# Performance work log

Measured on AMD Instinct MI355X. Metric: run time of the kernel, lower is better.

Reference implementation:

```python
import jax, jax.numpy as jnp
import numpy as np

NUM_HEADS = 16

def setup_inputs() -> dict:
    key = jax.random.key(0)
    k_x, k_wq, k_bq, k_wo, k_bo = jax.random.split(key, 5)
    B, S, D = 4, 2048, 1024
    x = jax.random.normal(k_x, (B, S, D), dtype=jnp.float32)
    # Flax Dense default init: lecun_normal for kernel, zeros for bias; use small normals here.
    w_qkv = jax.random.normal(k_wq, (D, 3 * D), dtype=jnp.float32) * (D ** -0.5)
    b_qkv = jnp.zeros((3 * D,), dtype=jnp.float32)
    w_out = jax.random.normal(k_wo, (D, D), dtype=jnp.float32) * (D ** -0.5)
    b_out = jnp.zeros((D,), dtype=jnp.float32)
    return {"x": x, "w_qkv": w_qkv, "b_qkv": b_qkv, "w_out": w_out, "b_out": b_out}

def reference(x, w_qkv, b_qkv, w_out, b_out):
    B, S, D = x.shape
    H = NUM_HEADS
    hd = D // H
    scale = hd ** -0.5
    qkv = x @ w_qkv + b_qkv                                  # [B,S,3D]
    qkv = qkv.reshape(B, S, 3, H, hd)
    qkv = jnp.transpose(qkv, (2, 0, 3, 1, 4))                # [3,B,H,S,hd]
    q, k, v = qkv[0], qkv[1], qkv[2]
    attn = jnp.einsum("bhqd,bhkd->bhqk", q, k) * scale       # [B,H,S,S]
    attn = jax.nn.softmax(attn, axis=-1)
    out = jnp.einsum("bhqk,bhkd->bhqd", attn, v)             # [B,H,S,hd]
    out = jnp.transpose(out, (0, 2, 1, 3)).reshape(B, S, D)
    return out @ w_out + b_out
```

## Files before the change

kernel.cpp:

```cpp
#include <hip/hip_runtime.h>
#include <cstdint>
#include <cstddef>

#define B_    4
#define S_    2048
#define D_    1024
#define H_    16
#define HD_   64
#define M_    8192
#define NQKV  3072

typedef __bf16 bf16;
typedef __bf16 bf16x4 __attribute__((ext_vector_type(4)));
typedef __bf16 bf16x8 __attribute__((ext_vector_type(8)));
typedef float  f32x2  __attribute__((ext_vector_type(2)));
typedef float  f32x4  __attribute__((ext_vector_type(4)));
typedef float  f32x16 __attribute__((ext_vector_type(16)));
typedef unsigned short u16x4 __attribute__((ext_vector_type(4)));
typedef uint32_t u32x2 __attribute__((ext_vector_type(2)));
typedef uint32_t u32x4 __attribute__((ext_vector_type(4)));

__device__ __forceinline__ void gl2lds16(const void* g, void* l) {
  __builtin_amdgcn_global_load_lds(
      (__attribute__((address_space(1))) void*)(uintptr_t)g,
      (__attribute__((address_space(3))) void*)l, 16, 0, 0);
}

__device__ __forceinline__ uint32_t pkbf16(float a, float b) {
  union { bf16 h[2]; uint32_t u; } z;
  z.h[0] = (bf16)a; z.h[1] = (bf16)b;
  return z.u;
}

__global__ __launch_bounds__(256) void cast_f32_bf16(const float* __restrict__ in,
                                                     bf16* __restrict__ out, int n4) {
  int i = blockIdx.x * 256 + threadIdx.x;
  if (i >= n4) return;
  float4 v = ((const float4*)in)[i];
  bf16x4 o;
  o[0] = (bf16)v.x; o[1] = (bf16)v.y; o[2] = (bf16)v.z; o[3] = (bf16)v.w;
  ((bf16x4*)out)[i] = o;
}

__global__ __launch_bounds__(256) void transpose_cast(const float* __restrict__ in,
                                                      bf16* __restrict__ out, int R, int C) {
  __shared__ float tile[32][33];
  int bx = blockIdx.x * 32, by = blockIdx.y * 32;
  int tx = threadIdx.x, ty = threadIdx.y;
#pragma unroll
  for (int i = 0; i < 32; i += 8)
    tile[ty + i][tx] = in[(size_t)(by + ty + i) * C + bx + tx];
  __syncthreads();
#pragma unroll
  for (int i = 0; i < 32; i += 8)
    out[(size_t)(bx + ty + i) * R + by + tx] = (bf16)tile[tx][ty + i];
}

template <bool OUT_BF16>
__global__ __launch_bounds__(256) void gemm_bt(const bf16* __restrict__ A,
                                               const bf16* __restrict__ Bt,
                                               const float* __restrict__ bias,
                                               void* __restrict__ Cptr,
                                               int M, int N, int K) {
  __shared__ __align__(16) bf16 As[128 * 64];
  __shared__ __align__(16) bf16 Bs[128 * 64];
  const int tid  = threadIdx.x;
  const int lane = tid & 63, w = tid >> 6;
  const int lo   = lane & 15, quad = lane >> 4;
  const int xcd = blockIdx.x & 7, g = blockIdx.x >> 3;
  const int mi  = g & 7,          n = g >> 3;
  const int bm  = (xcd * 8 + mi) * 128, bn = n * 128;
  const int wm = (w >> 1) * 64,    wn = (w & 1) * 64;

  f32x4 acc[4][4];
  const f32x4 zero = {0.f, 0.f, 0.f, 0.f};
#pragma unroll
  for (int i = 0; i < 4; ++i)
#pragma unroll
    for (int j = 0; j < 4; ++j) acc[i][j] = zero;

  for (int k0 = 0; k0 < K; k0 += 64) {
#pragma unroll
    for (int c = 0; c < 4; ++c) {
      int seg = c * 4 + w;
      int idx = seg * 512 + lane * 8;
      int row = idx >> 6, col = idx & 63;
      gl2lds16(A  + (size_t)(bm + row) * K + k0 + col, As + seg * 512);
      gl2lds16(Bt + (size_t)(bn + row) * K + k0 + col, Bs + seg * 512);
    }
    __syncthreads();
#pragma unroll
    for (int ks = 0; ks < 2; ++ks) {
      bf16x8 av[4], bv[4];
#pragma unroll
      for (int i = 0; i < 4; ++i)
        av[i] = *(const bf16x8*)&As[(wm + i * 16 + lo) * 64 + ks * 32 + quad * 8];
#pragma unroll
      for (int j = 0; j < 4; ++j)
        bv[j] = *(const bf16x8*)&Bs[(wn + j * 16 + lo) * 64 + ks * 32 + quad * 8];
#pragma unroll
      for (int i = 0; i < 4; ++i)
#pragma unroll
        for (int j = 0; j < 4; ++j)
          acc[i][j] = __builtin_amdgcn_mfma_f32_16x16x32_bf16(av[i], bv[j], acc[i][j], 0, 0, 0);
    }
    __syncthreads();
  }
#pragma unroll
  for (int j = 0; j < 4; ++j) {
    int cg = bn + wn + j * 16 + lo;
    float bsv = bias[cg];
#pragma unroll
    for (int i = 0; i < 4; ++i) {
      int rg = bm + wm + i * 16 + quad * 4;
#pragma unroll
      for (int r = 0; r < 4; ++r) {
        float v = acc[i][j][r] + bsv;
        if (OUT_BF16) ((bf16*)Cptr)[(size_t)(rg + r) * N + cg] = (bf16)v;
        else          ((float*)Cptr)[(size_t)(rg + r) * N + cg] = v;
      }
    }
  }
}

__global__ __launch_bounds__(256, 2) void gemm_bt_wide(const bf16* __restrict__ A,
                                                       const bf16* __restrict__ Bt,
                                                       const float* __restrict__ bias,
                                                       bf16* __restrict__ Cptr,
                                                       int M, int N, int K) {
  __shared__ __align__(16) bf16 As[128 * 64];
  __shared__ __align__(16) bf16 Bs[256 * 64];
  const int tid  = threadIdx.x;
  const int lane = tid & 63, w = tid >> 6;
  const int lo   = lane & 15, quad = lane >> 4;
  const int xcd = blockIdx.x & 7, g = blockIdx.x >> 3;
  const int mi  = g & 7,          n = g >> 3;
  const int bm  = (xcd * 8 + mi) * 128, bn = n * 256;
  const int wm = (w >> 1) * 64,    wn = (w & 1) * 128;

  f32x4 acc[4][8];
  const f32x4 zero = {0.f, 0.f, 0.f, 0.f};
#pragma unroll
  for (int i = 0; i < 4; ++i)
#pragma unroll
    for (int j = 0; j < 8; ++j) acc[i][j] = zero;

  for (int k0 = 0; k0 < K; k0 += 64) {
#pragma unroll
    for (int c = 0; c < 4; ++c) {
      int seg = c * 4 + w;
      int idx = seg * 512 + lane * 8;
      int row = idx >> 6, col = idx & 63;
      gl2lds16(A + (size_t)(bm + row) * K + k0 + col, As + seg * 512);
    }
#pragma unroll
    for (int c = 0; c < 8; ++c) {
      int seg = c * 4 + w;
      int idx = seg * 512 + lane * 8;
      int row = idx >> 6, col = idx & 63;
      gl2lds16(Bt + (size_t)(bn + row) * K + k0 + col, Bs + seg * 512);
    }
    __syncthreads();
#pragma unroll
    for (int ks = 0; ks < 2; ++ks) {
      bf16x8 av[4], bv[8];
#pragma unroll
      for (int i = 0; i < 4; ++i)
        av[i] = *(const bf16x8*)&As[(wm + i * 16 + lo) * 64 + ks * 32 + quad * 8];
#pragma unroll
      for (int j = 0; j < 8; ++j)
        bv[j] = *(const bf16x8*)&Bs[(wn + j * 16 + lo) * 64 + ks * 32 + quad * 8];
#pragma unroll
      for (int i = 0; i < 4; ++i)
#pragma unroll
        for (int j = 0; j < 8; ++j)
          acc[i][j] = __builtin_amdgcn_mfma_f32_16x16x32_bf16(av[i], bv[j], acc[i][j], 0, 0, 0);
    }
    __syncthreads();
  }
#pragma unroll
  for (int j = 0; j < 8; ++j) {
    int cg = bn + wn + j * 16 + lo;
    float bsv = bias[cg];
#pragma unroll
    for (int i = 0; i < 4; ++i) {
      int rg = bm + wm + i * 16 + quad * 4;
#pragma unroll
      for (int r = 0; r < 4; ++r)
        Cptr[(size_t)(rg + r) * N + cg] = (bf16)(acc[i][j][r] + bsv);
    }
  }
}

__global__ __launch_bounds__(256, 2) void flash_attn(const bf16* __restrict__ qkv,
                                                     bf16* __restrict__ out) {
  __shared__ __align__(16) bf16 smem[16384];
  bf16* const Ksm = smem;
  bf16* const Vsm = smem + 8192;

  const int tid  = threadIdx.x;
  const int lane = tid & 63, wq = tid >> 6;
  const int l31  = lane & 31;
  const int e    = lane >> 5;
  const int hi8  = e * 8, hi4 = e * 4;

  const int bid = blockIdx.x;
  const int qb  = bid >> 6;
  const int bh  = bid & 63;
  const int h   = bh & 15;
  const int b   = bh >> 4;
  const int q0  = qb * 256;
  const size_t rowb = (size_t)b * S_;
  const bf16* qbase = qkv + rowb * NQKV + h * HD_;
  const bf16* kbase = qbase + D_;
  const bf16* vbase = qbase + 2 * D_;

  bf16x8 qfA[4], qfB[4];
  {
    const bf16* qrow0 = qbase + (size_t)(q0 + wq * 64 + l31) * NQKV;
    const bf16* qrow1 = qrow0 + (size_t)32 * NQKV;
#pragma unroll
    for (int c = 0; c < 4; ++c) {
      qfA[c] = *(const bf16x8*)(qrow0 + c * 16 + hi8);
      qfB[c] = *(const bf16x8*)(qrow1 + c * 16 + hi8);
    }
  }

  int kq_off[2];
#pragma unroll
  for (int it = 0; it < 2; ++it) {
    int ci = it * 256 + tid;
    int s  = ci >> 3;
    int x  = (ci & 7) ^ (s & 7);
    kq_off[it] = s * NQKV + x * 8;
  }
  int vs_d[2], vs_s[2], vs_off[2];
#pragma unroll
  for (int u = 0; u < 2; ++u) {
    int idx = u * 256 + tid;
    int d0 = (idx & 31) * 2;
    int s0 = (idx >> 5) * 4;
    vs_d[u] = d0;
    vs_s[u] = s0;
    vs_off[u] = (((s0 >> 3) ^ ((d0 >> 1) & 7)) * 8) + (s0 & 7);
  }

  uint32_t vreg[2][4];

#pragma unroll
  for (int it = 0; it < 2; ++it)
    gl2lds16(kbase + kq_off[it], Ksm + (it * 256 + wq * 64) * 8);
#pragma unroll
  for (int u = 0; u < 2; ++u)
#pragma unroll
    for (int j = 0; j < 4; ++j)
      vreg[u][j] = *(const uint32_t*)(vbase + (size_t)(vs_s[u] + j) * NQKV + vs_d[u]);

  const f32x16 zero16 = {0.f,0.f,0.f,0.f,0.f,0.f,0.f,0.f,0.f,0.f,0.f,0.f,0.f,0.f,0.f,0.f};
  f32x16 oacc[2][2];
  oacc[0][0] = zero16; oacc[0][1] = zero16;
  oacc[1][0] = zero16; oacc[1][1] = zero16;
  f32x2 psA = {0.f, 0.f}, psB = {0.f, 0.f};
  const float c2 = 0.125f * 1.44269504088896341f;

  for (int kt = 0; kt < 32; ++kt) {
    const int buf = kt & 1;
#pragma unroll
    for (int u = 0; u < 2; ++u) {
      int d0 = vs_d[u];
      uint32_t lo0 = __builtin_amdgcn_perm(vreg[u][1], vreg[u][0], 0x05040100u);
      uint32_t lo1 = __builtin_amdgcn_perm(vreg[u][3], vreg[u][2], 0x05040100u);
      uint32_t hi0 = __builtin_amdgcn_perm(vreg[u][1], vreg[u][0], 0x07060302u);
      uint32_t hi1 = __builtin_amdgcn_perm(vreg[u][3], vreg[u][2], 0x07060302u);
      u32x2 lov = {lo0, lo1}, hiv = {hi0, hi1};
      *(u32x2*)&Vsm[buf * 4096 + (d0 + 0) * 64 + vs_off[u]] = lov;
      *(u32x2*)&Vsm[buf * 4096 + (d0 + 1) * 64 + vs_off[u]] = hiv;
    }
    __syncthreads();

    {
      int ktn = (kt + 1 < 32) ? kt + 1 : 31;
      const bf16* kb = kbase + (size_t)ktn * 64 * NQKV;
#pragma unroll
      for (int it = 0; it < 2; ++it)
        gl2lds16(kb + kq_off[it], Ksm + (buf ^ 1) * 4096 + (it * 256 + wq * 64) * 8);
    }
    {
      int ktn = (kt + 1 < 32) ? kt + 1 : 31;
      const bf16* vb = vbase + (size_t)ktn * 64 * NQKV;
#pragma unroll
      for (int u = 0; u < 2; ++u)
#pragma unroll
        for (int j = 0; j < 4; ++j)
          vreg[u][j] = *(const uint32_t*)(vb + (size_t)(vs_s[u] + j) * NQKV + vs_d[u]);
    }

#pragma unroll
    for (int kk = 0; kk < 2; ++kk) {
      f32x16 sA = zero16, sB = zero16;
      int srow = kk * 32 + l31;
      int swz  = (srow & 7) * 8;
#pragma unroll
      for (int c = 0; c < 4; ++c) {
        bf16x8 kf = *(const bf16x8*)&Ksm[buf * 4096 + srow * 64 + ((c * 16 + hi8) ^ swz)];
        sA = __builtin_amdgcn_mfma_f32_32x32x16_bf16(kf, qfA[c], sA, 0, 0, 0);
        sB = __builtin_amdgcn_mfma_f32_32x32x16_bf16(kf, qfB[c], sB, 0, 0, 0);
      }

      uint32_t Q8a[8], Q8b[8];
#pragma unroll
      for (int i = 0; i < 8; ++i) {
        f32x2 sva, svb;
        sva[0] = sA[2 * i]; sva[1] = sA[2 * i + 1];
        svb[0] = sB[2 * i]; svb[1] = sB[2 * i + 1];
        f32x2 ta = sva * c2 - 16.0f;
        f32x2 tb = svb * c2 - 16.0f;
        float a0 = __builtin_amdgcn_exp2f(ta[0]);
        float a1 = __builtin_amdgcn_exp2f(ta[1]);
        float b0 = __builtin_amdgcn_exp2f(tb[0]);
        float b1 = __builtin_amdgcn_exp2f(tb[1]);
        psA += (f32x2){a0, a1};
        psB += (f32x2){b0, b1};
        Q8a[i] = pkbf16(a0, a1);
        Q8b[i] = pkbf16(b0, b1);
      }

#pragma unroll
      for (int mh = 0; mh < 2; ++mh) {
        const int m = kk * 2 + mh, bq = mh * 4;
        u32x4 pda, pdb;
#if __has_builtin(__builtin_amdgcn_permlane32_swap)
        u32x2 wa0 = __builtin_amdgcn_permlane32_swap(Q8a[bq],     Q8a[bq + 2], false, false);
        u32x2 wa1 = __builtin_amdgcn_permlane32_swap(Q8a[bq + 1], Q8a[bq + 3], false, false);
        pda[0] = wa0[0]; pda[1] = wa1[0]; pda[2] = wa0[1]; pda[3] = wa1[1];
        u32x2 wb0 = __builtin_amdgcn_permlane32_swap(Q8b[bq],     Q8b[bq + 2], false, false);
        u32x2 wb1 = __builtin_amdgcn_permlane32_swap(Q8b[bq + 1], Q8b[bq + 3], false, false);
        pdb[0] = wb0[0]; pdb[1] = wb1[0]; pdb[2] = wb0[1]; pdb[3] = wb1[1];
#else
        {
          uint32_t s0 = e ? Q8a[bq]     : Q8a[bq + 2];
          uint32_t s1 = e ? Q8a[bq + 1] : Q8a[bq + 3];
          uint32_t r0 = __shfl_xor(s0, 32);
          uint32_t r1 = __shfl_xor(s1, 32);
          pda[0] = e ? r0 : Q8a[bq];
          pda[1] = e ? r1 : Q8a[bq + 1];
          pda[2] = e ? Q8a[bq + 2] : r0;
          pda[3] = e ? Q8a[bq + 3] : r1;
        }
        {
          uint32_t s0 = e ? Q8b[bq]     : Q8b[bq + 2];
          uint32_t s1 = e ? Q8b[bq + 1] : Q8b[bq + 3];
          uint32_t r0 = __shfl_xor(s0, 32);
          uint32_t r1 = __shfl_xor(s1, 32);
          pdb[0] = e ? r0 : Q8b[bq];
          pdb[1] = e ? r1 : Q8b[bq + 1];
          pdb[2] = e ? Q8b[bq + 2] : r0;
          pdb[3] = e ? Q8b[bq + 3] : r1;
        }
#endif
        bf16x8 pfa = __builtin_bit_cast(bf16x8, pda);
        bf16x8 pfb = __builtin_bit_cast(bf16x8, pdb);
#pragma unroll
        for (int dt = 0; dt < 2; ++dt) {
          int drow = dt * 32 + l31;
          int swv  = (drow >> 1) & 7;
          bf16x8 vf = *(const bf16x8*)&Vsm[buf * 4096 + drow * 64 + (((m * 2 + e) ^ swv) * 8)];
          oacc[dt][0] = __builtin_amdgcn_mfma_f32_32x32x16_bf16(vf, pfa, oacc[dt][0], 0, 0, 0);
          oacc[dt][1] = __builtin_amdgcn_mfma_f32_32x32x16_bf16(vf, pfb, oacc[dt][1], 0, 0, 0);
        }
      }
    }
  }

  float lsumA = psA[0] + psA[1];
  float lsumB = psB[0] + psB[1];
  lsumA += __shfl_xor(lsumA, 32);
  lsumB += __shfl_xor(lsumB, 32);

  __syncthreads();
  bf16* Os = smem;
  {
    float invA = 1.f / lsumA;
    float invB = 1.f / lsumB;
#pragma unroll
    for (int qs = 0; qs < 2; ++qs) {
      float inv = qs ? invB : invA;
      int ql = wq * 64 + qs * 32 + l31;
      int swO = (ql >> 1) & 7;
#pragma unroll
      for (int dt = 0; dt < 2; ++dt) {
#pragma unroll
        for (int g = 0; g < 4; ++g) {
          bf16x4 ov;
#pragma unroll
          for (int jj = 0; jj < 4; ++jj)
            ov[jj] = (bf16)(oacc[dt][qs][g * 4 + jj] * inv);
          *(bf16x4*)&Os[ql * 64 + (((dt * 4 + g) ^ swO) * 8) + hi4] = ov;
        }
      }
    }
  }
  __syncthreads();
#pragma unroll
  for (int it = 0; it < 8; ++it) {
    int idx = it * 256 + tid;
    int row = idx >> 3, c8 = idx & 7;
    bf16x8 t = *(const bf16x8*)&Os[row * 64 + ((c8 ^ ((row >> 1) & 7)) * 8)];
    *(bf16x8*)&out[(rowb + q0 + row) * D_ + h * HD_ + c8 * 8] = t;
  }
}

extern "C" void kernel_launch(void* const* d_in, const int* in_sizes, int n_in,
                              void* d_out, int out_size, void* d_ws, size_t ws_size,
                              hipStream_t stream) {
  const float* x     = (const float*)d_in[0];
  const float* w_qkv = (const float*)d_in[1];
  const float* b_qkv = (const float*)d_in[2];
  const float* w_out = (const float*)d_in[3];
  const float* b_out = (const float*)d_in[4];
  float* out = (float*)d_out;

  char* ws = (char*)d_ws;
  bf16* xb    = (bf16*)(ws);
  bf16* wqkvT = (bf16*)(ws + (size_t)16777216);
  bf16* woutT = (bf16*)(ws + (size_t)23068672);
  bf16* qkvb  = (bf16*)(ws + (size_t)25165824);
  bf16* attnb = (bf16*)(ws + (size_t)75497472);

  cast_f32_bf16<<<(M_ * D_ / 4 + 255) / 256, 256, 0, stream>>>(x, xb, M_ * D_ / 4);
  transpose_cast<<<dim3(NQKV / 32, D_ / 32), dim3(32, 8), 0, stream>>>(w_qkv, wqkvT, D_, NQKV);
  transpose_cast<<<dim3(D_ / 32, D_ / 32), dim3(32, 8), 0, stream>>>(w_out, woutT, D_, D_);

  gemm_bt_wide<<<(M_ / 128) * (NQKV / 256), 256, 0, stream>>>(
      xb, wqkvT, b_qkv, qkvb, M_, NQKV, D_);

  flash_attn<<<B_ * H_ * (S_ / 256), 256, 0, stream>>>(qkvb, attnb);

  gemm_bt<false><<<(M_ / 128) * (D_ / 128), 256, 0, stream>>>(
      attnb, woutT, b_out, (void*)out, M_, D_, D_);
}
```

Baseline: 283.2 us.

## Replace both GEMMs with triple-buffered 256x128 swizzled pipelined kernel and add MFMA priority

Both projection GEMMs now use one new kernel with 512 threads and a 256x128 output tile. It keeps a three-stage ring of tiles in LDS with an XOR swizzle. Global-to-LDS loads for the tile two steps ahead are split across the four MFMA phases and gated by vmcnt waits and barriers. This is meant to hide load latency and avoid LDS bank conflicts. s_setprio is also raised around the MFMA sections in both the GEMM and the flash attention kernel. The cost is 144KB of dynamic LDS, which allows only one block per CU, plus more frequent barriers.

```diff
diff --git a/kernel.cpp b/kernel.cpp
--- a/kernel.cpp
+++ b/kernel.cpp
@@ -16,9 +16,10 @@
 typedef float  f32x2  __attribute__((ext_vector_type(2)));
 typedef float  f32x4  __attribute__((ext_vector_type(4)));
 typedef float  f32x16 __attribute__((ext_vector_type(16)));
-typedef unsigned short u16x4 __attribute__((ext_vector_type(4)));
 typedef uint32_t u32x2 __attribute__((ext_vector_type(2)));
 typedef uint32_t u32x4 __attribute__((ext_vector_type(4)));
+
+#define MFMA16(a, b, c) __builtin_amdgcn_mfma_f32_16x16x32_bf16(a, b, c, 0, 0, 0)
 
 __device__ __forceinline__ void gl2lds16(const void* g, void* l) {
   __builtin_amdgcn_global_load_lds(
@@ -57,20 +58,41 @@
 }
 
 template <bool OUT_BF16>
-__global__ __launch_bounds__(256) void gemm_bt(const bf16* __restrict__ A,
-                                               const bf16* __restrict__ Bt,
-                                               const float* __restrict__ bias,
-                                               void* __restrict__ Cptr,
-                                               int M, int N, int K) {
-  __shared__ __align__(16) bf16 As[128 * 64];
-  __shared__ __align__(16) bf16 Bs[128 * 64];
+__global__ __launch_bounds__(512, 2) void gemm256(const bf16* __restrict__ A,
+                                                  const bf16* __restrict__ Bt,
+                                                  const float* __restrict__ bias,
+                                                  void* __restrict__ Cptr,
+                                                  int M, int N, int K) {
+  extern __shared__ __align__(16) bf16 sm[];
   const int tid  = threadIdx.x;
   const int lane = tid & 63, w = tid >> 6;
   const int lo   = lane & 15, quad = lane >> 4;
-  const int xcd = blockIdx.x & 7, g = blockIdx.x >> 3;
-  const int mi  = g & 7,          n = g >> 3;
-  const int bm  = (xcd * 8 + mi) * 128, bn = n * 128;
-  const int wm = (w >> 1) * 64,    wn = (w & 1) * 64;
+  const int wr   = w >> 1, wc = w & 1;
+  const int xcd  = blockIdx.x & 7, g = blockIdx.x >> 3;
+  const int mi_  = g & 3, n_ = g >> 2;
+  const int bm   = (xcd * 4 + mi_) * 256, bn = n_ * 128;
+
+  const bf16* Ag = A  + (size_t)bm * K;
+  const bf16* Bg = Bt + (size_t)bn * K;
+
+  const int swzl  = lo & 7;
+  const int laneA = (wr * 64 + lo) * 64;
+  const int laneB = (wc * 64 + lo) * 64;
+  const int pc0   = (quad ^ swzl) * 8;
+  const int pc1   = ((4 + quad) ^ swzl) * 8;
+
+  int aoffG[4], boffG[2];
+#pragma unroll
+  for (int la = 0; la < 4; ++la) {
+    int ca = la * 512 + tid, row = ca >> 3, s = ca & 7;
+    aoffG[la] = row * K + ((s ^ (row & 7)) * 8);
+  }
+#pragma unroll
+  for (int lb = 0; lb < 2; ++lb) {
+    int cb = lb * 512 + tid, row = cb >> 3, s = cb & 7;
+    boffG[lb] = row * K + ((s ^ (row & 7)) * 8);
+  }
+  const int T = K >> 6;
 
   f32x4 acc[4][4];
   const f32x4 zero = {0.f, 0.f, 0.f, 0.f};
@@ -79,115 +101,116 @@
 #pragma unroll
     for (int j = 0; j < 4; ++j) acc[i][j] = zero;
 
-  for (int k0 = 0; k0 < K; k0 += 64) {
-#pragma unroll
-    for (int c = 0; c < 4; ++c) {
-      int seg = c * 4 + w;
-      int idx = seg * 512 + lane * 8;
-      int row = idx >> 6, col = idx & 63;
-      gl2lds16(A  + (size_t)(bm + row) * K + k0 + col, As + seg * 512);
-      gl2lds16(Bt + (size_t)(bn + row) * K + k0 + col, Bs + seg * 512);
-    }
-    __syncthreads();
-#pragma unroll
-    for (int ks = 0; ks < 2; ++ks) {
-      bf16x8 av[4], bv[4];
-#pragma unroll
-      for (int i = 0; i < 4; ++i)
-        av[i] = *(const bf16x8*)&As[(wm + i * 16 + lo) * 64 + ks * 32 + quad * 8];
-#pragma unroll
-      for (int j = 0; j < 4; ++j)
-        bv[j] = *(const bf16x8*)&Bs[(wn + j * 16 + lo) * 64 + ks * 32 + quad * 8];
-#pragma unroll
-      for (int i = 0; i < 4; ++i)
-#pragma unroll
-        for (int j = 0; j < 4; ++j)
-          acc[i][j] = __builtin_amdgcn_mfma_f32_16x16x32_bf16(av[i], bv[j], acc[i][j], 0, 0, 0);
-    }
-    __syncthreads();
-  }
+#pragma unroll
+  for (int la = 0; la < 4; ++la)
+    gl2lds16(Ag + aoffG[la], sm + (la * 512 + tid) * 8);
+#pragma unroll
+  for (int lb = 0; lb < 2; ++lb)
+    gl2lds16(Bg + boffG[lb], sm + 16384 + (lb * 512 + tid) * 8);
+#pragma unroll
+  for (int la = 0; la < 4; ++la)
+    gl2lds16(Ag + 64 + aoffG[la], sm + 24576 + (la * 512 + tid) * 8);
+#pragma unroll
+  for (int lb = 0; lb < 2; ++lb)
+    gl2lds16(Bg + 64 + boffG[lb], sm + 24576 + 16384 + (lb * 512 + tid) * 8);
+  asm volatile("s_waitcnt vmcnt(6)" ::: "memory");
+  __builtin_amdgcn_s_barrier();
+
+  auto body = [&](int t, bool st) __attribute__((always_inline)) {
+    bf16* As_ = sm + (t % 3) * 24576;
+    bf16* Bs_ = As_ + 16384;
+    bf16* An_ = sm + ((t + 2) % 3) * 24576;
+    bf16* Bn_ = An_ + 16384;
+    const size_t kg = (size_t)(t + 2) * 64;
+    bf16x8 av0, av1, bv[4];
+
+    av0 = *(const bf16x8*)&As_[laneA + 0 * 1024 + pc0];
+    av1 = *(const bf16x8*)&As_[laneA + 1 * 1024 + pc0];
+#pragma unroll
+    for (int j = 0; j < 4; ++j)
+      bv[j] = *(const bf16x8*)&Bs_[laneB + j * 1024 + pc0];
+    if (st) {
+      gl2lds16(Ag + kg + aoffG[0], An_ + (0 * 512 + tid) * 8);
+      gl2lds16(Ag + kg + aoffG[1], An_ + (1 * 512 + tid) * 8);
+    }
+    __builtin_amdgcn_s_barrier();
+    __builtin_amdgcn_s_setprio(1);
+#pragma unroll
+    for (int j = 0; j < 4; ++j) {
+      acc[0][j] = MFMA16(av0, bv[j], acc[0][j]);
+      acc[1][j] = MFMA16(av1, bv[j], acc[1][j]);
+    }
+    __builtin_amdgcn_s_setprio(0);
+
+    av0 = *(const bf16x8*)&As_[laneA + 2 * 1024 + pc0];
+    av1 = *(const bf16x8*)&As_[laneA + 3 * 1024 + pc0];
+    if (st) {
+      gl2lds16(Ag + kg + aoffG[2], An_ + (2 * 512 + tid) * 8);
+      gl2lds16(Ag + kg + aoffG[3], An_ + (3 * 512 + tid) * 8);
+    }
+    __builtin_amdgcn_s_barrier();
+    __builtin_amdgcn_s_setprio(1);
+#pragma unroll
+    for (int j = 0; j < 4; ++j) {
+      acc[2][j] = MFMA16(av0, bv[j], acc[2][j]);
+      acc[3][j] = MFMA16(av1, bv[j], acc[3][j]);
+    }
+    __builtin_amdgcn_s_setprio(0);
+
+    av0 = *(const bf16x8*)&As_[laneA + 0 * 1024 + pc1];
+    av1 = *(const bf16x8*)&As_[laneA + 1 * 1024 + pc1];
+#pragma unroll
+    for (int j = 0; j < 4; ++j)
+      bv[j] = *(const bf16x8*)&Bs_[laneB + j * 1024 + pc1];
+    if (st)
+      gl2lds16(Bg + kg + boffG[0], Bn_ + (0 * 512 + tid) * 8);
+    __builtin_amdgcn_s_barrier();
+    __builtin_amdgcn_s_setprio(1);
+#pragma unroll
+    for (int j = 0; j < 4; ++j) {
+      acc[0][j] = MFMA16(av0, bv[j], acc[0][j]);
+      acc[1][j] = MFMA16(av1, bv[j], acc[1][j]);
+    }
+    __builtin_amdgcn_s_setprio(0);
+
+    av0 = *(const bf16x8*)&As_[laneA + 2 * 1024 + pc1];
+    av1 = *(const bf16x8*)&As_[laneA + 3 * 1024 + pc1];
+    if (st)
+      gl2lds16(Bg + kg + boffG[1], Bn_ + (1 * 512 + tid) * 8);
+    __builtin_amdgcn_s_barrier();
+    __builtin_amdgcn_s_setprio(1);
+#pragma unroll
+    for (int j = 0; j < 4; ++j) {
+      acc[2][j] = MFMA16(av0, bv[j], acc[2][j]);
+      acc[3][j] = MFMA16(av1, bv[j], acc[3][j]);
+    }
+    __builtin_amdgcn_s_setprio(0);
+  };
+
+#pragma unroll 1
+  for (int t = 0; t < T - 2; ++t) {
+    body(t, true);
+    asm volatile("s_waitcnt vmcnt(6)" ::: "memory");
+    __builtin_amdgcn_s_barrier();
+  }
+  body(T - 2, false);
+  asm volatile("s_waitcnt vmcnt(0)" ::: "memory");
+  __builtin_amdgcn_s_barrier();
+  body(T - 1, false);
+
 #pragma unroll
   for (int j = 0; j < 4; ++j) {
-    int cg = bn + wn + j * 16 + lo;
+    int cg = bn + wc * 64 + j * 16 + lo;
     float bsv = bias[cg];
 #pragma unroll
     for (int i = 0; i < 4; ++i) {
-      int rg = bm + wm + i * 16 + quad * 4;
+      int rg = bm + wr * 64 + i * 16 + quad * 4;
 #pragma unroll
       for (int r = 0; r < 4; ++r) {
         float v = acc[i][j][r] + bsv;
         if (OUT_BF16) ((bf16*)Cptr)[(size_t)(rg + r) * N + cg] = (bf16)v;
         else          ((float*)Cptr)[(size_t)(rg + r) * N + cg] = v;
       }
-    }
-  }
-}
-
-__global__ __launch_bounds__(256, 2) void gemm_bt_wide(const bf16* __restrict__ A,
-                                                       const bf16* __restrict__ Bt,
-                                                       const float* __restrict__ bias,
-                                                       bf16* __restrict__ Cptr,
-                                                       int M, int N, int K) {
-  __shared__ __align__(16) bf16 As[128 * 64];
-  __shared__ __align__(16) bf16 Bs[256 * 64];
-  const int tid  = threadIdx.x;
-  const int lane = tid & 63, w = tid >> 6;
-  const int lo   = lane & 15, quad = lane >> 4;
-  const int xcd = blockIdx.x & 7, g = blockIdx.x >> 3;
-  const int mi  = g & 7,          n = g >> 3;
-  const int bm  = (xcd * 8 + mi) * 128, bn = n * 256;
-  const int wm = (w >> 1) * 64,    wn = (w & 1) * 128;
-
-  f32x4 acc[4][8];
-  const f32x4 zero = {0.f, 0.f, 0.f, 0.f};
-#pragma unroll
-  for (int i = 0; i < 4; ++i)
-#pragma unroll
-    for (int j = 0; j < 8; ++j) acc[i][j] = zero;
-
-  for (int k0 = 0; k0 < K; k0 += 64) {
-#pragma unroll
-    for (int c = 0; c < 4; ++c) {
-      int seg = c * 4 + w;
-      int idx = seg * 512 + lane * 8;
-      int row = idx >> 6, col = idx & 63;
-      gl2lds16(A + (size_t)(bm + row) * K + k0 + col, As + seg * 512);
-    }
-#pragma unroll
-    for (int c = 0; c < 8; ++c) {
-      int seg = c * 4 + w;
-      int idx = seg * 512 + lane * 8;
-      int row = idx >> 6, col = idx & 63;
-      gl2lds16(Bt + (size_t)(bn + row) * K + k0 + col, Bs + seg * 512);
-    }
-    __syncthreads();
-#pragma unroll
-    for (int ks = 0; ks < 2; ++ks) {
-      bf16x8 av[4], bv[8];
-#pragma unroll
-      for (int i = 0; i < 4; ++i)
-        av[i] = *(const bf16x8*)&As[(wm + i * 16 + lo) * 64 + ks * 32 + quad * 8];
-#pragma unroll
-      for (int j = 0; j < 8; ++j)
-        bv[j] = *(const bf16x8*)&Bs[(wn + j * 16 + lo) * 64 + ks * 32 + quad * 8];
-#pragma unroll
-      for (int i = 0; i < 4; ++i)
-#pragma unroll
-        for (int j = 0; j < 8; ++j)
-          acc[i][j] = __builtin_amdgcn_mfma_f32_16x16x32_bf16(av[i], bv[j], acc[i][j], 0, 0, 0);
-    }
-    __syncthreads();
-  }
-#pragma unroll
-  for (int j = 0; j < 8; ++j) {
-    int cg = bn + wn + j * 16 + lo;
-    float bsv = bias[cg];
-#pragma unroll
-    for (int i = 0; i < 4; ++i) {
-      int rg = bm + wm + i * 16 + quad * 4;
-#pragma unroll
-      for (int r = 0; r < 4; ++r)
-        Cptr[(size_t)(rg + r) * N + cg] = (bf16)(acc[i][j][r] + bsv);
     }
   }
 }
@@ -300,12 +323,14 @@
       f32x16 sA = zero16, sB = zero16;
       int srow = kk * 32 + l31;
       int swz  = (srow & 7) * 8;
+      __builtin_amdgcn_s_setprio(1);
 #pragma unroll
       for (int c = 0; c < 4; ++c) {
         bf16x8 kf = *(const bf16x8*)&Ksm[buf * 4096 + srow * 64 + ((c * 16 + hi8) ^ swz)];
         sA = __builtin_amdgcn_mfma_f32_32x32x16_bf16(kf, qfA[c], sA, 0, 0, 0);
         sB = __builtin_amdgcn_mfma_f32_32x32x16_bf16(kf, qfB[c], sB, 0, 0, 0);
       }
+      __builtin_amdgcn_s_setprio(0);
 
       uint32_t Q8a[8], Q8b[8];
 #pragma unroll
@@ -360,6 +385,7 @@
 #endif
         bf16x8 pfa = __builtin_bit_cast(bf16x8, pda);
         bf16x8 pfb = __builtin_bit_cast(bf16x8, pdb);
+        __builtin_amdgcn_s_setprio(1);
 #pragma unroll
         for (int dt = 0; dt < 2; ++dt) {
           int drow = dt * 32 + l31;
@@ -368,6 +394,7 @@
           oacc[dt][0] = __builtin_amdgcn_mfma_f32_32x32x16_bf16(vf, pfa, oacc[dt][0], 0, 0, 0);
           oacc[dt][1] = __builtin_amdgcn_mfma_f32_32x32x16_bf16(vf, pfb, oacc[dt][1], 0, 0, 0);
         }
+        __builtin_amdgcn_s_setprio(0);
       }
     }
   }
@@ -427,15 +454,24 @@
   bf16* qkvb  = (bf16*)(ws + (size_t)25165824);
   bf16* attnb = (bf16*)(ws + (size_t)75497472);
 
+  static int attr_done = 0;
+  if (!attr_done) {
+    hipFuncSetAttribute(reinterpret_cast<const void*>(&gemm256<true>),
+                        hipFuncAttributeMaxDynamicSharedMemorySize, 147456);
+    hipFuncSetAttribute(reinterpret_cast<const void*>(&gemm256<false>),
+                        hipFuncAttributeMaxDynamicSharedMemorySize, 147456);
+    attr_done = 1;
+  }
+
   cast_f32_bf16<<<(M_ * D_ / 4 + 255) / 256, 256, 0, stream>>>(x, xb, M_ * D_ / 4);
   transpose_cast<<<dim3(NQKV / 32, D_ / 32), dim3(32, 8), 0, stream>>>(w_qkv, wqkvT, D_, NQKV);
   transpose_cast<<<dim3(D_ / 32, D_ / 32), dim3(32, 8), 0, stream>>>(w_out, woutT, D_, D_);
 
-  gemm_bt_wide<<<(M_ / 128) * (NQKV / 256), 256, 0, stream>>>(
-      xb, wqkvT, b_qkv, qkvb, M_, NQKV, D_);
+  gemm256<true><<<(M_ / 256) * (NQKV / 128), 512, 147456, stream>>>(
+      xb, wqkvT, b_qkv, (void*)qkvb, M_, NQKV, D_);
 
   flash_attn<<<B_ * H_ * (S_ / 256), 256, 0, stream>>>(qkvb, attnb);
 
-  gemm_bt<false><<<(M_ / 128) * (D_ / 128), 256, 0, stream>>>(
+  gemm256<false><<<(M_ / 256) * (D_ / 128), 512, 147456, stream>>>(
       attnb, woutT, b_out, (void*)out, M_, D_, D_);
 }
```

Result: faster. 273.3 us (-3.5%).
